# Kernel optimization log

Measured on AMD Instinct MI355X. Metric: run time of the kernel, lower is better.

Reference implementation:

```python
import jax, jax.numpy as jnp
import numpy as np

N = 2048  # num_nodes


def setup_inputs() -> dict:
    key = jax.random.key(0)
    adj_matrix = jax.random.normal(key, (N, N), dtype=jnp.float32)
    return {"adj_matrix": adj_matrix, "source_node": 0}


def reference(adj_matrix, source_node):
    # Faithful vectorization of the torch triple loop.
    # Within outer iteration i, every relaxation reads only column i-1 and
    # writes column i (which starts at +inf), so column i is exactly
    #   dist[v, i] = min_u (dist[u, i-1] + adj[u, v])
    # and predecessors[v, i] is the FIRST u attaining that min (strict-< update
    # rule => first argmin; if the min is inf no update fires and pred stays 0,
    # which argmin over an all-inf column also yields).
    n = adj_matrix.shape[0]
    d0 = jnp.full((n,), jnp.inf, dtype=adj_matrix.dtype).at[source_node].set(0.0)

    def step(d_prev, _):
        cand = d_prev[:, None] + adj_matrix          # [u, v]
        d_new = jnp.min(cand, axis=0)                # [v]
        pred = jnp.argmin(cand, axis=0).astype(jnp.int32)
        return d_new, (d_new, pred)

    _, (ds, preds) = jax.lax.scan(step, d0, None, length=n - 1)

    # distances[v, i]: column 0 is the init column, columns 1..n-1 from the scan.
    distances = jnp.concatenate([d0[None, :], ds], axis=0).T          # [n, n]
    predecessors = jnp.concatenate(
        [jnp.zeros((1, n), jnp.int32), preds], axis=0
    ).T                                                               # [n, n]

    d_last = distances[:, n - 1]
    has_negative_cycle = jnp.any(d_last[:, None] + adj_matrix < d_last[None, :])
    return (distances, predecessors, has_negative_cycle)
```

## Files before the change

### kernel.cpp

```cpp
#include <hip/hip_runtime.h>

#define NN   2048
#define NBLK 256
#define TPB  512
#define CPB  8
#define SENT 1.0e30f

typedef unsigned long long u64;

struct BFWS {
  u64 pub[2][NN];
  u64 cyc[NBLK];
};

__device__ __forceinline__ u64 ld64(u64* p) {
  return __hip_atomic_load(p, __ATOMIC_RELAXED, __HIP_MEMORY_SCOPE_AGENT);
}
__device__ __forceinline__ void st64(u64* p, u64 v) {
  __hip_atomic_store(p, v, __ATOMIC_RELAXED, __HIP_MEMORY_SCOPE_AGENT);
}

__device__ __forceinline__ float wave_min64_dpp(float x) {
  int v = __float_as_int(x);
  #define BF_STAGE(ctrl)                                                   \
    { int tdpp = __builtin_amdgcn_update_dpp(v, v, ctrl, 0xf, 0xf, false); \
      v = __float_as_int(fminf(__int_as_float(v), __int_as_float(tdpp))); }
  BF_STAGE(0x111)
  BF_STAGE(0x112)
  BF_STAGE(0x114)
  BF_STAGE(0x118)
  BF_STAGE(0x142)
  BF_STAGE(0x143)
  #undef BF_STAGE
  return __int_as_float(v);
}

__global__ void bf_init(BFWS* ws) {
  int t = threadIdx.x;
  if (t < NBLK) ws->cyc[t] = 0ull;
}

__global__ void __launch_bounds__(TPB, 1)
bf_main(const float* __restrict__ A, const int* __restrict__ srcp,
        float* __restrict__ dist, float* __restrict__ pred,
        float* __restrict__ flagout, BFWS* ws) {
  const int tid = threadIdx.x;
  const int b   = blockIdx.x;
  const int c   = tid >> 6;
  const int s   = tid & 63;
  const int col = b * CPB + c;
  const int src = srcp[0];

  __shared__ __align__(16) float d_lds[2][NN];
  __shared__ int bflag;

  float a[32];
  #pragma unroll
  for (int k = 0; k < 8; ++k) {
    #pragma unroll
    for (int m = 0; m < 4; ++m) {
      int i = 4 * (s + 64 * k) + m;
      a[4 * k + m] = A[(size_t)i * NN + col];
    }
  }

  #pragma unroll
  for (int h = 0; h < 4; ++h) {
    int e = h * TPB + tid;
    d_lds[0][e] = (e == src) ? 0.f : SENT;
  }
  if (s == 0) {
    dist[(size_t)col * NN] = (col == src) ? 0.f : SENT;
    pred[(size_t)col * NN] = 0.f;
  }
  __syncthreads();

  for (int t = 1; t <= NN - 1; ++t) {
    if (t > 1) {
      u64* pb = ws->pub[(t - 1) & 1] + 4 * tid;
      const unsigned want = (unsigned)(t - 1);
      u64 v[4];
      unsigned got = 0;
      while (got != 0xFu) {
        #pragma unroll
        for (int h = 0; h < 4; ++h)
          if (!((got >> h) & 1)) v[h] = ld64(pb + h);
        #pragma unroll
        for (int h = 0; h < 4; ++h)
          if (!((got >> h) & 1) && (unsigned)(v[h] >> 32) == want) got |= 1u << h;
        if (got != 0xFu) __builtin_amdgcn_s_sleep(1);
      }
      float4 f;
      f.x = __uint_as_float((unsigned)v[0]);
      f.y = __uint_as_float((unsigned)v[1]);
      f.z = __uint_as_float((unsigned)v[2]);
      f.w = __uint_as_float((unsigned)v[3]);
      *reinterpret_cast<float4*>(&d_lds[(t - 1) & 1][4 * tid]) = f;
      __syncthreads();
    }

    float bv0 = 2.f * SENT, bv1 = 2.f * SENT, bv2 = 2.f * SENT, bv3 = 2.f * SENT;
    int   bi0 = 0,          bi1 = 1,          bi2 = 2,          bi3 = 3;
    const float4* dq4 = reinterpret_cast<const float4*>(d_lds[(t - 1) & 1]);
    #pragma unroll
    for (int k = 0; k < 8; ++k) {
      float4 dq = dq4[s + 64 * k];
      int base = 4 * (s + 64 * k);
      float c0 = dq.x + a[4 * k + 0];
      float c1 = dq.y + a[4 * k + 1];
      float c2 = dq.z + a[4 * k + 2];
      float c3 = dq.w + a[4 * k + 3];
      if (c0 < bv0) { bv0 = c0; bi0 = base + 0; }
      if (c1 < bv1) { bv1 = c1; bi1 = base + 1; }
      if (c2 < bv2) { bv2 = c2; bi2 = base + 2; }
      if (c3 < bv3) { bv3 = c3; bi3 = base + 3; }
    }

    float mv = wave_min64_dpp(fminf(fminf(bv0, bv1), fminf(bv2, bv3)));
    if (s == 63)
      st64(&ws->pub[t & 1][col], ((u64)(unsigned)t << 32) | (u64)__float_as_uint(mv));

    float bv = bv0; int bi = bi0;
    if (bv1 < bv || (bv1 == bv && bi1 < bi)) { bv = bv1; bi = bi1; }
    if (bv2 < bv || (bv2 == bv && bi2 < bi)) { bv = bv2; bi = bi2; }
    if (bv3 < bv || (bv3 == bv && bi3 < bi)) { bv = bv3; bi = bi3; }
    #pragma unroll
    for (int off = 32; off; off >>= 1) {
      float ov = __shfl_xor(bv, off, 64);
      int   oi = __shfl_xor(bi, off, 64);
      if (ov < bv || (ov == bv && oi < bi)) { bv = ov; bi = oi; }
    }
    if (s == 1) {
      dist[(size_t)col * NN + t] = bv;
      pred[(size_t)col * NN + t] = (float)bi;
    }
  }

  {
    u64* pb = ws->pub[(NN - 1) & 1] + 4 * tid;
    const unsigned want = (unsigned)(NN - 1);
    u64 v[4];
    unsigned got = 0;
    while (got != 0xFu) {
      #pragma unroll
      for (int h = 0; h < 4; ++h)
        if (!((got >> h) & 1)) v[h] = ld64(pb + h);
      #pragma unroll
      for (int h = 0; h < 4; ++h)
        if (!((got >> h) & 1) && (unsigned)(v[h] >> 32) == want) got |= 1u << h;
      if (got != 0xFu) __builtin_amdgcn_s_sleep(1);
    }
    float4 f;
    f.x = __uint_as_float((unsigned)v[0]);
    f.y = __uint_as_float((unsigned)v[1]);
    f.z = __uint_as_float((unsigned)v[2]);
    f.w = __uint_as_float((unsigned)v[3]);
    *reinterpret_cast<float4*>(&d_lds[1][4 * tid]) = f;
    if (tid == 0) bflag = 0;
    __syncthreads();

    float dj = d_lds[1][col];
    int viol = 0;
    const float4* dq4 = reinterpret_cast<const float4*>(d_lds[1]);
    #pragma unroll
    for (int k = 0; k < 8; ++k) {
      float4 dq = dq4[s + 64 * k];
      viol |= (dq.x + a[4 * k + 0] < dj);
      viol |= (dq.y + a[4 * k + 1] < dj);
      viol |= (dq.z + a[4 * k + 2] < dj);
      viol |= (dq.w + a[4 * k + 3] < dj);
    }
    if (viol) bflag = 1;
    __syncthreads();
    if (tid == 0)
      st64(&ws->cyc[b], ((u64)(unsigned)NN << 32) | (u64)(unsigned)bflag);
  }

  if (b == 0) {
    int myv = 0;
    if (tid < NBLK) {
      u64 w;
      do {
        w = ld64(&ws->cyc[tid]);
        if ((unsigned)(w >> 32) == (unsigned)NN) break;
        __builtin_amdgcn_s_sleep(1);
      } while (true);
      myv = (int)((unsigned)w & 1u);
    }
    if (tid == 0) bflag = 0;
    __syncthreads();
    if (myv) bflag = 1;
    __syncthreads();
    if (tid == 0) flagout[0] = bflag ? 1.f : 0.f;
  }
}

extern "C" void kernel_launch(void* const* d_in, const int* in_sizes, int n_in,
                              void* d_out, int out_size, void* d_ws, size_t ws_size,
                              hipStream_t stream) {
  (void)in_sizes; (void)n_in; (void)out_size; (void)ws_size;
  const float* A    = (const float*)d_in[0];
  const int*   srcp = (const int*)d_in[1];
  float* dist    = (float*)d_out;
  float* pred    = dist + (size_t)NN * NN;
  float* flagout = dist + (size_t)2 * NN * NN;
  BFWS*  ws      = (BFWS*)d_ws;

  bf_init<<<1, 256, 0, stream>>>(ws);
  bf_main<<<dim3(NBLK), dim3(TPB), 0, stream>>>(A, srcp, dist, pred, flagout, ws);
}
```

Baseline: 4.335 ms.

## Halve block count with 1024-thread blocks and poll pairs via system-coherent dwordx4 loads

```diff
diff --git a/kernel.cpp b/kernel.cpp
--- a/kernel.cpp
+++ b/kernel.cpp
@@ -1,12 +1,13 @@
 #include <hip/hip_runtime.h>
 
 #define NN   2048
-#define NBLK 256
-#define TPB  512
-#define CPB  8
+#define NBLK 128
+#define TPB  1024
+#define CPB  16
 #define SENT 1.0e30f
 
 typedef unsigned long long u64;
+typedef __attribute__((ext_vector_type(4))) unsigned int u32x4;
 
 struct BFWS {
   u64 pub[2][NN];
@@ -18,6 +19,13 @@
 }
 __device__ __forceinline__ void st64(u64* p, u64 v) {
   __hip_atomic_store(p, v, __ATOMIC_RELAXED, __HIP_MEMORY_SCOPE_AGENT);
+}
+__device__ __forceinline__ u32x4 ld_pair_mall(const u64* p) {
+  u32x4 r;
+  asm volatile("global_load_dwordx4 %0, %1, off sc0 sc1\n\t"
+               "s_waitcnt vmcnt(0)"
+               : "=&v"(r) : "v"(p) : "memory");
+  return r;
 }
 
 __device__ __forceinline__ float wave_min64_dpp(float x) {
@@ -64,10 +72,12 @@
     }
   }
 
-  #pragma unroll
-  for (int h = 0; h < 4; ++h) {
-    int e = h * TPB + tid;
-    d_lds[0][e] = (e == src) ? 0.f : SENT;
+  {
+    int e = 2 * tid;
+    float2 f;
+    f.x = (e + 0 == src) ? 0.f : SENT;
+    f.y = (e + 1 == src) ? 0.f : SENT;
+    *reinterpret_cast<float2*>(&d_lds[0][e]) = f;
   }
   if (s == 0) {
     dist[(size_t)col * NN] = (col == src) ? 0.f : SENT;
@@ -77,25 +87,18 @@
 
   for (int t = 1; t <= NN - 1; ++t) {
     if (t > 1) {
-      u64* pb = ws->pub[(t - 1) & 1] + 4 * tid;
+      const u64* pb = ws->pub[(t - 1) & 1] + 2 * tid;
       const unsigned want = (unsigned)(t - 1);
-      u64 v[4];
-      unsigned got = 0;
-      while (got != 0xFu) {
-        #pragma unroll
-        for (int h = 0; h < 4; ++h)
-          if (!((got >> h) & 1)) v[h] = ld64(pb + h);
-        #pragma unroll
-        for (int h = 0; h < 4; ++h)
-          if (!((got >> h) & 1) && (unsigned)(v[h] >> 32) == want) got |= 1u << h;
-        if (got != 0xFu) __builtin_amdgcn_s_sleep(1);
+      u32x4 r;
+      for (;;) {
+        r = ld_pair_mall(pb);
+        if ((r.y == want) & (r.w == want)) break;
+        __builtin_amdgcn_s_sleep(1);
       }
-      float4 f;
-      f.x = __uint_as_float((unsigned)v[0]);
-      f.y = __uint_as_float((unsigned)v[1]);
-      f.z = __uint_as_float((unsigned)v[2]);
-      f.w = __uint_as_float((unsigned)v[3]);
-      *reinterpret_cast<float4*>(&d_lds[(t - 1) & 1][4 * tid]) = f;
+      float2 f;
+      f.x = __uint_as_float(r.x);
+      f.y = __uint_as_float(r.z);
+      *reinterpret_cast<float2*>(&d_lds[(t - 1) & 1][2 * tid]) = f;
       __syncthreads();
     }
 
@@ -137,25 +140,18 @@
   }
 
   {
-    u64* pb = ws->pub[(NN - 1) & 1] + 4 * tid;
+    const u64* pb = ws->pub[1] + 2 * tid;
     const unsigned want = (unsigned)(NN - 1);
-    u64 v[4];
-    unsigned got = 0;
-    while (got != 0xFu) {
-      #pragma unroll
-      for (int h = 0; h < 4; ++h)
-        if (!((got >> h) & 1)) v[h] = ld64(pb + h);
-      #pragma unroll
-      for (int h = 0; h < 4; ++h)
-        if (!((got >> h) & 1) && (unsigned)(v[h] >> 32) == want) got |= 1u << h;
-      if (got != 0xFu) __builtin_amdgcn_s_sleep(1);
-    }
-    float4 f;
-    f.x = __uint_as_float((unsigned)v[0]);
-    f.y = __uint_as_float((unsigned)v[1]);
-    f.z = __uint_as_float((unsigned)v[2]);
-    f.w = __uint_as_float((unsigned)v[3]);
-    *reinterpret_cast<float4*>(&d_lds[1][4 * tid]) = f;
+    u32x4 r;
+    for (;;) {
+      r = ld_pair_mall(pb);
+      if ((r.y == want) & (r.w == want)) break;
+      __builtin_amdgcn_s_sleep(1);
+    }
+    float2 f;
+    f.x = __uint_as_float(r.x);
+    f.y = __uint_as_float(r.z);
+    *reinterpret_cast<float2*>(&d_lds[1][2 * tid]) = f;
     if (tid == 0) bflag = 0;
     __syncthreads();
 
@@ -187,6 +183,7 @@
       } while (true);
       myv = (int)((unsigned)w & 1u);
     }
+    __syncthreads();
     if (tid == 0) bflag = 0;
     __syncthreads();
     if (myv) bflag = 1;
```

Result: slower. 4.937 ms (+13.9%).
